# Kernel optimization log

Measured on AMD Instinct MI355X. Metric: run time of the kernel, lower is better.

The kernel has to match this reference:

```python
import jax, jax.numpy as jnp
import numpy as np

B, T, W, D, NT = 32, 512, 250, 768, 2  # batch, subtokens, words, sim_dim, num_tags


def setup_inputs() -> dict:
    key = jax.random.key(0)
    ks = jax.random.split(key, 20)
    s = 0.05
    # words_ids: 2 subtokens per word for W words, rest padding (-100)
    pos = jnp.arange(T)
    wid = jnp.where(pos < 2 * W, pos // 2, -100).astype(jnp.int64)
    words_ids = jnp.broadcast_to(wid, (B, T))
    inp = {
        'bert_out': jax.random.normal(ks[0], (B, T, D), jnp.float32),
        'words_ids': words_ids,
        'label_detect': jax.random.randint(ks[1], (B, W), 0, NT).astype(jnp.int64),
        'w_ih_l0': jax.random.normal(ks[2], (4 * D, D), jnp.float32) * s,
        'w_hh_l0': jax.random.normal(ks[3], (4 * D, D), jnp.float32) * s,
        'b_l0': jax.random.normal(ks[4], (4 * D,), jnp.float32) * s,
        'w_ih_l0r': jax.random.normal(ks[5], (4 * D, D), jnp.float32) * s,
        'w_hh_l0r': jax.random.normal(ks[6], (4 * D, D), jnp.float32) * s,
        'b_l0r': jax.random.normal(ks[7], (4 * D,), jnp.float32) * s,
        'w_ih_l1': jax.random.normal(ks[8], (4 * D, 2 * D), jnp.float32) * s,
        'w_hh_l1': jax.random.normal(ks[9], (4 * D, D), jnp.float32) * s,
        'b_l1': jax.random.normal(ks[10], (4 * D,), jnp.float32) * s,
        'w_ih_l1r': jax.random.normal(ks[11], (4 * D, 2 * D), jnp.float32) * s,
        'w_hh_l1r': jax.random.normal(ks[12], (4 * D, D), jnp.float32) * s,
        'b_l1r': jax.random.normal(ks[13], (4 * D,), jnp.float32) * s,
        'w_lin': jax.random.normal(ks[14], (NT, 2 * D), jnp.float32) * s,
        'b_lin': jax.random.normal(ks[15], (NT,), jnp.float32) * s,
        'crf_start': jax.random.normal(ks[16], (NT,), jnp.float32) * 0.1,
        'crf_end': jax.random.normal(ks[17], (NT,), jnp.float32) * 0.1,
        'crf_trans': jax.random.normal(ks[18], (NT, NT), jnp.float32) * 0.1,
    }
    return inp


def first_subtoken_gather(bert_out, words_ids):
    # For each word w in [0, W): embedding of its FIRST subtoken.
    # (matches torch.unique(sorted)+first-element-per-group on HF word_ids)
    pos = jnp.arange(T)
    mask = words_ids[:, None, :] == jnp.arange(W)[None, :, None]  # [B, W, T]
    first_idx = jnp.min(jnp.where(mask, pos[None, None, :], T - 1), axis=-1)  # [B, W]
    return jnp.take_along_axis(bert_out, first_idx[..., None], axis=1)  # [B, W, D]


def lstm_dir(x, w_ih, w_hh, b, reverse):
    # x: [B, S, In] -> [B, S, H]; PyTorch gate order i, f, g, o
    H = w_hh.shape[1]
    pre = jnp.einsum('bsi,gi->bsg', x, w_ih) + b  # b = b_ih + b_hh
    if reverse:
        pre = pre[:, ::-1]
    def step(carry, p_t):
        h, c = carry
        g = p_t + h @ w_hh.T
        i, f, gg, o = jnp.split(g, 4, axis=-1)
        c = jax.nn.sigmoid(f) * c + jax.nn.sigmoid(i) * jnp.tanh(gg)
        h = jax.nn.sigmoid(o) * jnp.tanh(c)
        return (h, c), h
    h0 = jnp.zeros((x.shape[0], H), x.dtype)
    _, hs = jax.lax.scan(step, (h0, h0), jnp.swapaxes(pre, 0, 1))
    hs = jnp.swapaxes(hs, 0, 1)
    if reverse:
        hs = hs[:, ::-1]
    return hs


def crf_log_likelihood(emis, tags, start, end, trans):
    # emis: [B, S, K]; tags: [B, S]; mask = all ones; reduction='mean'
    S = emis.shape[1]
    # numerator
    t0 = tags[:, 0]
    emis_score = jnp.sum(jnp.take_along_axis(emis, tags[..., None], axis=-1)[..., 0], axis=1)
    trans_score = jnp.sum(trans[tags[:, :-1], tags[:, 1:]], axis=1)
    num = start[t0] + emis_score + trans_score + end[tags[:, -1]]
    # partition (forward algorithm)
    alpha0 = start[None, :] + emis[:, 0]  # [B, K]
    def step(alpha, e_t):
        alpha = jax.nn.logsumexp(alpha[:, :, None] + trans[None] + e_t[:, None, :], axis=1)
        return alpha, None
    alpha, _ = jax.lax.scan(step, alpha0, jnp.swapaxes(emis[:, 1:], 0, 1))
    logZ = jax.nn.logsumexp(alpha + end[None, :], axis=-1)
    return jnp.mean(num - logZ)


def crf_decode(emis, start, end, trans):
    # Viterbi, mask = all ones. Returns [B, S] int32.
    score0 = start[None, :] + emis[:, 0]
    def fwd(score, e_t):
        cand = score[:, :, None] + trans[None]          # [B, K, K]
        bp = jnp.argmax(cand, axis=1)                    # [B, K]
        score = jnp.max(cand, axis=1) + e_t
        return score, bp
    score, hist = jax.lax.scan(fwd, score0, jnp.swapaxes(emis[:, 1:], 0, 1))
    last = jnp.argmax(score + end[None, :], axis=-1)     # [B]
    def back(tag, bp_t):
        prev = jnp.take_along_axis(bp_t, tag[:, None], axis=1)[:, 0]
        return prev, prev
    _, prevs = jax.lax.scan(back, last, hist, reverse=True)
    path = jnp.concatenate([jnp.swapaxes(prevs, 0, 1), last[:, None]], axis=1)
    return path.astype(jnp.int32)


def reference(bert_out, words_ids, label_detect,
              w_ih_l0, w_hh_l0, b_l0, w_ih_l0r, w_hh_l0r, b_l0r,
              w_ih_l1, w_hh_l1, b_l1, w_ih_l1r, w_hh_l1r, b_l1r,
              w_lin, b_lin, crf_start, crf_end, crf_trans):
    feat = first_subtoken_gather(bert_out, words_ids)                      # [B, W, D]
    h1 = jnp.concatenate([lstm_dir(feat, w_ih_l0, w_hh_l0, b_l0, False),
                          lstm_dir(feat, w_ih_l0r, w_hh_l0r, b_l0r, True)], axis=-1)
    h2 = jnp.concatenate([lstm_dir(h1, w_ih_l1, w_hh_l1, b_l1, False),
                          lstm_dir(h1, w_ih_l1r, w_hh_l1r, b_l1r, True)], axis=-1)
    logits = h2 @ w_lin.T + b_lin                                           # [B, W, 2]
    ner_prob = jax.nn.softmax(logits, axis=-1)
    llh = crf_log_likelihood(ner_prob, label_detect, crf_start, crf_end, crf_trans)
    path = crf_decode(ner_prob, crf_start, crf_end, crf_trans)
    loss = -1.0 * llh
    return path, ner_prob, loss
```

## Files before the change

kernel.cpp:

```cpp
#include <hip/hip_runtime.h>
#include <cmath>

#define B_ 32
#define T_ 512
#define W_ 250
#define D_ 768
#define H_ 768
#define G_ 3072
#define NT_ 2

#define NBAR_ 1152

__global__ void first_idx_kernel(const int* __restrict__ words_ids, int* __restrict__ fidx,
                                 unsigned int* __restrict__ counter) {
  int i = blockIdx.x * blockDim.x + threadIdx.x;
  if (i < NBAR_) counter[i] = 0u;
  if (i >= B_ * W_) return;
  int b = i / W_, w = i % W_;
  const int* row = words_ids + (size_t)b * T_;
  int idx = T_ - 1;
  for (int t = 0; t < T_; ++t) {
    if (row[t] == w) { idx = t; break; }
  }
  fidx[i] = idx;
}

__global__ void gather_kernel(const float* __restrict__ bert_out, const int* __restrict__ fidx,
                              float* __restrict__ feat) {
  int i = blockIdx.x * blockDim.x + threadIdx.x;
  const int nv = D_ / 4;
  if (i >= B_ * W_ * nv) return;
  int bw = i / nv, d4 = i % nv;
  int b = bw / W_, w = bw % W_;
  int t = fidx[bw];
  float4 v = ((const float4*)(bert_out + ((size_t)b * T_ + t) * D_))[d4];
  ((float4*)(feat + ((size_t)w * B_ + b) * D_))[d4] = v;
}

__global__ __launch_bounds__(256) void gemm_bias_kernel(
    const float* __restrict__ A, const float* __restrict__ Bm,
    const float* __restrict__ bias, float* __restrict__ C,
    int M, int N, int K) {
  __shared__ float As[2][16][132];
  __shared__ float Bs[2][16][132];
  const int tid = threadIdx.x;
  const int row0 = blockIdx.x * 128;
  const int col0 = blockIdx.y * 128;
  const int tx = tid & 15;
  const int ty = tid >> 4;
  const int lr = tid >> 1;
  const int lk = (tid & 1) * 8;

  int ar = row0 + lr;
  if (ar >= M) ar = M - 1;
  const float* __restrict__ Ap = A + (size_t)ar * K + lk;
  const float* __restrict__ Bp = Bm + (size_t)(col0 + lr) * K + lk;

  float acc[8][8];
#pragma unroll
  for (int i = 0; i < 8; ++i)
#pragma unroll
    for (int j = 0; j < 8; ++j) acc[i][j] = 0.0f;

  const int nk = K >> 4;

  {
    float4 a0 = *(const float4*)(Ap + 0);
    float4 a1 = *(const float4*)(Ap + 4);
    float4 b0 = *(const float4*)(Bp + 0);
    float4 b1 = *(const float4*)(Bp + 4);
    As[0][lk + 0][lr] = a0.x; As[0][lk + 1][lr] = a0.y; As[0][lk + 2][lr] = a0.z; As[0][lk + 3][lr] = a0.w;
    As[0][lk + 4][lr] = a1.x; As[0][lk + 5][lr] = a1.y; As[0][lk + 6][lr] = a1.z; As[0][lk + 7][lr] = a1.w;
    Bs[0][lk + 0][lr] = b0.x; Bs[0][lk + 1][lr] = b0.y; Bs[0][lk + 2][lr] = b0.z; Bs[0][lk + 3][lr] = b0.w;
    Bs[0][lk + 4][lr] = b1.x; Bs[0][lk + 5][lr] = b1.y; Bs[0][lk + 6][lr] = b1.z; Bs[0][lk + 7][lr] = b1.w;
  }
  __syncthreads();

  for (int t = 0; t < nk; ++t) {
    const int cur = t & 1;
    float4 a0, a1, b0, b1;
    const bool pf = (t + 1 < nk);
    if (pf) {
      const int k0 = (t + 1) << 4;
      a0 = *(const float4*)(Ap + k0);
      a1 = *(const float4*)(Ap + k0 + 4);
      b0 = *(const float4*)(Bp + k0);
      b1 = *(const float4*)(Bp + k0 + 4);
    }
#pragma unroll
    for (int k = 0; k < 16; ++k) {
      float a[8], b[8];
      *(float4*)&a[0] = *(const float4*)&As[cur][k][ty * 8];
      *(float4*)&a[4] = *(const float4*)&As[cur][k][ty * 8 + 4];
      *(float4*)&b[0] = *(const float4*)&Bs[cur][k][tx * 8];
      *(float4*)&b[4] = *(const float4*)&Bs[cur][k][tx * 8 + 4];
#pragma unroll
      for (int i = 0; i < 8; ++i)
#pragma unroll
        for (int j = 0; j < 8; ++j) acc[i][j] += a[i] * b[j];
    }
    if (pf) {
      const int nxt = cur ^ 1;
      As[nxt][lk + 0][lr] = a0.x; As[nxt][lk + 1][lr] = a0.y; As[nxt][lk + 2][lr] = a0.z; As[nxt][lk + 3][lr] = a0.w;
      As[nxt][lk + 4][lr] = a1.x; As[nxt][lk + 5][lr] = a1.y; As[nxt][lk + 6][lr] = a1.z; As[nxt][lk + 7][lr] = a1.w;
      Bs[nxt][lk + 0][lr] = b0.x; Bs[nxt][lk + 1][lr] = b0.y; Bs[nxt][lk + 2][lr] = b0.z; Bs[nxt][lk + 3][lr] = b0.w;
      Bs[nxt][lk + 4][lr] = b1.x; Bs[nxt][lk + 5][lr] = b1.y; Bs[nxt][lk + 6][lr] = b1.z; Bs[nxt][lk + 7][lr] = b1.w;
    }
    __syncthreads();
  }

#pragma unroll
  for (int i = 0; i < 8; ++i) {
    int r = row0 + ty * 8 + i;
    if (r < M) {
#pragma unroll
      for (int j = 0; j < 8; ++j) {
        int c = col0 + tx * 8 + j;
        C[(size_t)r * N + c] = acc[i][j] + bias[c];
      }
    }
  }
}

__global__ __launch_bounds__(256) void lstm_persist_kernel(
    const float* __restrict__ pre_f, const float* __restrict__ pre_r,
    const float* __restrict__ whh_f, const float* __restrict__ whh_r,
    float* __restrict__ out, float* __restrict__ hbuf, float* __restrict__ cbuf,
    unsigned int* __restrict__ counter, int s0, int Cc, int ep0) {
  const int wg = blockIdx.x;
  const int dir = wg >> 7;
  const int lw = wg & 127;
  const float* __restrict__ pre = dir ? pre_r : pre_f;
  const float* __restrict__ whh = dir ? whh_r : whh_f;
  float* hb = hbuf + (size_t)dir * 2 * B_ * H_;
  float* cb = cbuf + (size_t)dir * B_ * H_;
  const int tid = threadIdx.x;
  const int u0 = lw * 6;

  const int rgrp = tid >> 6;
  const int lane = tid & 63;
  const int kgrp = lane >> 3;
  const int bgrp = lane & 7;

  __shared__ float w_lds[24 * 860];
  __shared__ float h_lds[32 * 284];
  __shared__ float g_lds[32][24];

  unsigned int* __restrict__ grp  = counter + ((wg & 7) << 6);
  unsigned int* __restrict__ root = counter + 512;
  unsigned int* __restrict__ gow  = counter + 576 + ((wg & 7) << 6);

#pragma unroll
  for (int v = 0; v < 18; ++v) {
    int i = v * 256 + tid;
    int r24 = i / 192;
    int f4 = i - r24 * 192;
    int k = f4 * 4;
    int grow = (r24 / 6) * H_ + u0 + (r24 % 6);
    *(float4*)&w_lds[r24 * 860 + k + 4 * (k >> 5)] =
        *(const float4*)(whh + (size_t)grow * H_ + k);
  }

  const int cui = tid >> 5;
  const int cb_ = tid & 31;
  float creg = 0.0f;
  if (tid < 192 && s0 > 0) creg = cb[(size_t)cb_ * H_ + u0 + cui];

  float pre_g0 = 0.f, pre_g1 = 0.f, pre_g2 = 0.f, pre_g3 = 0.f;
  if (tid < 192) {
    const int prow0 = dir ? (Cc - 1) : 0;
    const float* pbt = pre + ((size_t)prow0 * B_ + cb_) * G_;
    pre_g0 = pbt[0 * H_ + u0 + cui];
    pre_g1 = pbt[1 * H_ + u0 + cui];
    pre_g2 = pbt[2 * H_ + u0 + cui];
    pre_g3 = pbt[3 * H_ + u0 + cui];
  }

  const int kl0 = kgrp * 32;

  for (int sl = 0; sl < Cc; ++sl) {
    const int s = s0 + sl;
    const int w = dir ? (W_ - 1 - s) : s;

    float acc[6][4];
#pragma unroll
    for (int r = 0; r < 6; ++r)
#pragma unroll
      for (int j = 0; j < 4; ++j) acc[r][j] = 0.0f;

    if (s > 0) {
      const float* __restrict__ hprev = hb + (size_t)(s & 1) * B_ * H_;

      unsigned long long hq[16];
#pragma unroll
      for (int v = 0; v < 8; ++v) {
        int e = v * 1024 + tid * 4;
        int bb = e >> 8;
        int kk = e & 255;
        const unsigned long long* src =
            (const unsigned long long*)(hprev + (size_t)bb * H_ + kk);
        hq[2 * v]     = __hip_atomic_load(src + 0, __ATOMIC_RELAXED, __HIP_MEMORY_SCOPE_AGENT);
        hq[2 * v + 1] = __hip_atomic_load(src + 1, __ATOMIC_RELAXED, __HIP_MEMORY_SCOPE_AGENT);
      }

      for (int kc = 0; kc < H_; kc += 256) {
        __syncthreads();
#pragma unroll
        for (int v = 0; v < 8; ++v) {
          int e = v * 1024 + tid * 4;
          int bb = e >> 8;
          int kk = e & 255;
          int off = bb * 284 + kk + 4 * (kk >> 5);
          union { unsigned long long u; float f[2]; } q0, q1;
          q0.u = hq[2 * v]; q1.u = hq[2 * v + 1];
          h_lds[off + 0] = q0.f[0]; h_lds[off + 1] = q0.f[1];
          h_lds[off + 2] = q1.f[0]; h_lds[off + 3] = q1.f[1];
        }
        __syncthreads();
        if (kc + 256 < H_) {
#pragma unroll
          for (int v = 0; v < 8; ++v) {
            int e = v * 1024 + tid * 4;
            int bb = e >> 8;
            int kk = e & 255;
            const unsigned long long* src =
                (const unsigned long long*)(hprev + (size_t)bb * H_ + kc + 256 + kk);
            hq[2 * v]     = __hip_atomic_load(src + 0, __ATOMIC_RELAXED, __HIP_MEMORY_SCOPE_AGENT);
            hq[2 * v + 1] = __hip_atomic_load(src + 1, __ATOMIC_RELAXED, __HIP_MEMORY_SCOPE_AGENT);
          }
        }

        const int wbase = kc + kl0;
#pragma unroll 4
        for (int t = 0; t < 8; ++t) {
          const int kl = kl0 + t * 4;
          const int ka = wbase + t * 4;
          const int hoff = kl + 4 * (kl >> 5);
          const int woff = ka + 4 * (ka >> 5);
          float4 h4_0 = *(const float4*)&h_lds[(4 * bgrp + 0) * 284 + hoff];
          float4 h4_1 = *(const float4*)&h_lds[(4 * bgrp + 1) * 284 + hoff];
          float4 h4_2 = *(const float4*)&h_lds[(4 * bgrp + 2) * 284 + hoff];
          float4 h4_3 = *(const float4*)&h_lds[(4 * bgrp + 3) * 284 + hoff];
#pragma unroll
          for (int r = 0; r < 6; ++r) {
            float4 w4 = *(const float4*)&w_lds[(rgrp * 6 + r) * 860 + woff];
            acc[r][0] += h4_0.x * w4.x + h4_0.y * w4.y + h4_0.z * w4.z + h4_0.w * w4.w;
            acc[r][1] += h4_1.x * w4.x + h4_1.y * w4.y + h4_1.z * w4.z + h4_1.w * w4.w;
            acc[r][2] += h4_2.x * w4.x + h4_2.y * w4.y + h4_2.z * w4.z + h4_2.w * w4.w;
            acc[r][3] += h4_3.x * w4.x + h4_3.y * w4.y + h4_3.z * w4.z + h4_3.w * w4.w;
          }
        }
      }

#pragma unroll
      for (int r = 0; r < 6; ++r)
#pragma unroll
        for (int j = 0; j < 4; ++j) {
          float a = acc[r][j];
          a += __shfl_xor(a, 8, 64);
          a += __shfl_xor(a, 16, 64);
          a += __shfl_xor(a, 32, 64);
          acc[r][j] = a;
        }
      if (kgrp == 0) {
#pragma unroll
        for (int r = 0; r < 6; ++r)
#pragma unroll
          for (int j = 0; j < 4; ++j)
            g_lds[4 * bgrp + j][rgrp * 6 + r] = acc[r][j];
      }
    }

    __syncthreads();

    if (tid < 192) {
      float gi = pre_g0, gf = pre_g1, gg = pre_g2, go = pre_g3;
      if (s > 0) {
        gi += g_lds[cb_][cui];
        gf += g_lds[cb_][6 + cui];
        gg += g_lds[cb_][12 + cui];
        go += g_lds[cb_][18 + cui];
      }
      const float si = 1.0f / (1.0f + expf(-gi));
      const float sf = 1.0f / (1.0f + expf(-gf));
      const float so = 1.0f / (1.0f + expf(-go));
      creg = sf * creg + si * tanhf(gg);
      const float h = so * tanhf(creg);
      float* __restrict__ hnext = hb + (size_t)((s + 1) & 1) * B_ * H_;
      __hip_atomic_store(&hnext[(size_t)cb_ * H_ + u0 + cui], h,
                         __ATOMIC_RELAXED, __HIP_MEMORY_SCOPE_AGENT);
      out[((size_t)w * B_ + cb_) * (2 * H_) + (size_t)dir * H_ + u0 + cui] = h;
      if (sl + 1 < Cc) {
        const int prown = dir ? (Cc - 2 - sl) : (sl + 1);
        const float* pbtn = pre + ((size_t)prown * B_ + cb_) * G_;
        pre_g0 = pbtn[0 * H_ + u0 + cui];
        pre_g1 = pbtn[1 * H_ + u0 + cui];
        pre_g2 = pbtn[2 * H_ + u0 + cui];
        pre_g3 = pbtn[3 * H_ + u0 + cui];
      }
    }

    __syncthreads();
    if (tid == 0) {
      const unsigned int ep1 = (unsigned int)(ep0 + sl + 1);
      unsigned int old = __hip_atomic_fetch_add(grp, 1u, __ATOMIC_RELAXED, __HIP_MEMORY_SCOPE_AGENT);
      if (old == 32u * ep1 - 1u) {
        __hip_atomic_fetch_add(root, 1u, __ATOMIC_RELAXED, __HIP_MEMORY_SCOPE_AGENT);
        while (__hip_atomic_load(root, __ATOMIC_RELAXED, __HIP_MEMORY_SCOPE_AGENT) < 8u * ep1) {
          __builtin_amdgcn_s_sleep(2);
        }
        __hip_atomic_store(gow, ep1, __ATOMIC_RELAXED, __HIP_MEMORY_SCOPE_AGENT);
      } else {
        while (__hip_atomic_load(gow, __ATOMIC_RELAXED, __HIP_MEMORY_SCOPE_AGENT) < ep1) {
          __builtin_amdgcn_s_sleep(2);
        }
      }
    }
    __syncthreads();
  }

  if (tid < 192) cb[(size_t)cb_ * H_ + u0 + cui] = creg;
}

__global__ void logits_softmax_kernel(const float* __restrict__ h2, const float* __restrict__ w_lin,
                                      const float* __restrict__ b_lin, float* __restrict__ prob) {
  int i = blockIdx.x * blockDim.x + threadIdx.x;
  if (i >= B_ * W_) return;
  int b = i / W_, w = i % W_;
  const float4* x = (const float4*)(h2 + ((size_t)w * B_ + b) * (2 * H_));
  const float4* w0 = (const float4*)(w_lin);
  const float4* w1 = (const float4*)(w_lin + 2 * H_);
  float l0 = 0.f, l1 = 0.f;
#pragma unroll 4
  for (int k = 0; k < (2 * H_) / 4; ++k) {
    float4 xv = x[k];
    float4 a = w0[k];
    float4 c = w1[k];
    l0 += xv.x * a.x + xv.y * a.y + xv.z * a.z + xv.w * a.w;
    l1 += xv.x * c.x + xv.y * c.y + xv.z * c.z + xv.w * c.w;
  }
  l0 += b_lin[0];
  l1 += b_lin[1];
  float m = fmaxf(l0, l1);
  float e0 = expf(l0 - m), e1 = expf(l1 - m);
  float s = e0 + e1;
  prob[2 * (size_t)i] = e0 / s;
  prob[2 * (size_t)i + 1] = e1 / s;
}

__device__ __forceinline__ float lse2(float a, float b) {
  float m = fmaxf(a, b);
  return m + logf(expf(a - m) + expf(b - m));
}

__global__ void crf_llh_kernel(const float* __restrict__ emis, const int* __restrict__ tags,
                               const float* __restrict__ start, const float* __restrict__ endv,
                               const float* __restrict__ trans, float* __restrict__ loss_out) {
  int tid = threadIdx.x;
  float val = 0.f;
  if (tid < B_) {
    const float* e = emis + (size_t)tid * W_ * NT_;
    const int* tg = tags + (size_t)tid * W_;
    const float t00 = trans[0], t01 = trans[1], t10 = trans[2], t11 = trans[3];
    int tp = tg[0];
    float num = start[tp] + e[tp];
    float a0 = start[0] + e[0];
    float a1 = start[1] + e[1];
    for (int s = 1; s < W_; ++s) {
      int ts = tg[s];
      num += e[2 * s + ts] + trans[tp * 2 + ts];
      tp = ts;
      float n0 = lse2(a0 + t00, a1 + t10) + e[2 * s];
      float n1 = lse2(a0 + t01, a1 + t11) + e[2 * s + 1];
      a0 = n0;
      a1 = n1;
    }
    num += endv[tp];
    float logZ = lse2(a0 + endv[0], a1 + endv[1]);
    val = num - logZ;
  }
  for (int off = 32; off > 0; off >>= 1) val += __shfl_down(val, off, 64);
  if (tid == 0) loss_out[0] = -(val / (float)B_);
}

__global__ void crf_decode_kernel(const float* __restrict__ emis,
                                  const float* __restrict__ start, const float* __restrict__ endv,
                                  const float* __restrict__ trans, float* __restrict__ path_out) {
  int b = blockIdx.x * blockDim.x + threadIdx.x;
  if (b >= B_) return;
  const float* e = emis + (size_t)b * W_ * NT_;
  const float t00 = trans[0], t01 = trans[1], t10 = trans[2], t11 = trans[3];
  float s0 = start[0] + e[0];
  float s1 = start[1] + e[1];
  unsigned long long bp0[4] = {0ull, 0ull, 0ull, 0ull};
  unsigned long long bp1[4] = {0ull, 0ull, 0ull, 0ull};
  for (int s = 1; s < W_; ++s) {
    float c00 = s0 + t00, c10 = s1 + t10;
    float c01 = s0 + t01, c11 = s1 + t11;
    int b0 = (c10 > c00) ? 1 : 0;
    int b1 = (c11 > c01) ? 1 : 0;
    float m0 = b0 ? c10 : c00;
    float m1 = b1 ? c11 : c01;
    int idx = s - 1;
    bp0[idx >> 6] |= ((unsigned long long)b0) << (idx & 63);
    bp1[idx >> 6] |= ((unsigned long long)b1) << (idx & 63);
    s0 = m0 + e[2 * s];
    s1 = m1 + e[2 * s + 1];
  }
  int tag = ((s1 + endv[1]) > (s0 + endv[0])) ? 1 : 0;
  path_out[(size_t)b * W_ + (W_ - 1)] = (float)tag;
  for (int s = W_ - 2; s >= 0; --s) {
    unsigned long long word = tag ? bp1[s >> 6] : bp0[s >> 6];
    tag = (int)((word >> (s & 63)) & 1ull);
    path_out[(size_t)b * W_ + s] = (float)tag;
  }
}

extern "C" void kernel_launch(void* const* d_in, const int* in_sizes, int n_in,
                              void* d_out, int out_size, void* d_ws, size_t ws_size,
                              hipStream_t stream) {
  const float* bert_out = (const float*)d_in[0];
  const int* words_ids = (const int*)d_in[1];
  const int* label_detect = (const int*)d_in[2];
  const float* w_ih_l0 = (const float*)d_in[3];
  const float* w_hh_l0 = (const float*)d_in[4];
  const float* b_l0 = (const float*)d_in[5];
  const float* w_ih_l0r = (const float*)d_in[6];
  const float* w_hh_l0r = (const float*)d_in[7];
  const float* b_l0r = (const float*)d_in[8];
  const float* w_ih_l1 = (const float*)d_in[9];
  const float* w_hh_l1 = (const float*)d_in[10];
  const float* b_l1 = (const float*)d_in[11];
  const float* w_ih_l1r = (const float*)d_in[12];
  const float* w_hh_l1r = (const float*)d_in[13];
  const float* b_l1r = (const float*)d_in[14];
  const float* w_lin = (const float*)d_in[15];
  const float* b_lin = (const float*)d_in[16];
  const float* crf_start = (const float*)d_in[17];
  const float* crf_end = (const float*)d_in[18];
  const float* crf_trans = (const float*)d_in[19];

  float* out = (float*)d_out;
  float* path_out = out;
  float* prob_out = out + B_ * W_;
  float* loss_out = out + B_ * W_ * 3;

  auto need = [](int c) -> size_t { return 4ull * (24732672ull + 196608ull * (size_t)c); };
  int C = 10;
  if (ws_size >= need(250)) C = 250;
  else if (ws_size >= need(125)) C = 125;
  else if (ws_size >= need(50)) C = 50;
  else if (ws_size >= need(25)) C = 25;
  const int nchunk = W_ / C;
  const size_t CBG = (size_t)C * B_ * G_;

  float* h2 = (float*)d_ws;
  float* feat = h2;
  float* h1 = h2 + 12288000;
  float* preA = h1 + 12288000;
  float* preB = preA + CBG;
  float* hbuf = preB + CBG;
  float* cbuf = hbuf + 2 * 2 * B_ * H_;
  int* fidx = (int*)(cbuf + 2 * B_ * H_);
  unsigned int* counter = (unsigned int*)(fidx + B_ * W_);

  first_idx_kernel<<<(B_ * W_ + 255) / 256, 256, 0, stream>>>(words_ids, fidx, counter);
  gather_kernel<<<(B_ * W_ * (D_ / 4) + 255) / 256, 256, 0, stream>>>(bert_out, fidx, feat);

  const int Mc = C * B_;
  dim3 ggrid((Mc + 127) / 128, G_ / 128);
  int ep = 0;

  for (int ch = 0; ch < nchunk; ++ch) {
    const int s0 = ch * C;
    gemm_bias_kernel<<<ggrid, 256, 0, stream>>>(feat + (size_t)s0 * B_ * D_, w_ih_l0, b_l0, preA, Mc, G_, D_);
    gemm_bias_kernel<<<ggrid, 256, 0, stream>>>(feat + (size_t)(W_ - C - s0) * B_ * D_, w_ih_l0r, b_l0r, preB, Mc, G_, D_);
    const float* a0 = preA; const float* a1 = preB;
    const float* a2 = w_hh_l0; const float* a3 = w_hh_l0r;
    float* a4 = h1; float* a5 = hbuf; float* a6 = cbuf;
    unsigned int* a7 = counter; int a8 = s0; int a9 = C; int a10 = ep;
    void* args[] = {&a0, &a1, &a2, &a3, &a4, &a5, &a6, &a7, &a8, &a9, &a10};
    hipLaunchCooperativeKernel((void*)lstm_persist_kernel, dim3(256), dim3(256), args, 0, stream);
    ep += C;
  }

  for (int ch = 0; ch < nchunk; ++ch) {
    const int s0 = ch * C;
    gemm_bias_kernel<<<ggrid, 256, 0, stream>>>(h1 + (size_t)s0 * B_ * (2 * H_), w_ih_l1, b_l1, preA, Mc, G_, 2 * H_);
    gemm_bias_kernel<<<ggrid, 256, 0, stream>>>(h1 + (size_t)(W_ - C - s0) * B_ * (2 * H_), w_ih_l1r, b_l1r, preB, Mc, G_, 2 * H_);
    const float* a0 = preA; const float* a1 = preB;
    const float* a2 = w_hh_l1; const float* a3 = w_hh_l1r;
    float* a4 = h2; float* a5 = hbuf; float* a6 = cbuf;
    unsigned int* a7 = counter; int a8 = s0; int a9 = C; int a10 = ep;
    void* args[] = {&a0, &a1, &a2, &a3, &a4, &a5, &a6, &a7, &a8, &a9, &a10};
    hipLaunchCooperativeKernel((void*)lstm_persist_kernel, dim3(256), dim3(256), args, 0, stream);
    ep += C;
  }

  logits_softmax_kernel<<<(B_ * W_ + 255) / 256, 256, 0, stream>>>(h2, w_lin, b_lin, prob_out);

  crf_llh_kernel<<<1, 64, 0, stream>>>(prob_out, label_detect, crf_start, crf_end, crf_trans, loss_out);
  crf_decode_kernel<<<1, 64, 0, stream>>>(prob_out, crf_start, crf_end, crf_trans, path_out);
}
```

Baseline: 10.81 ms.

## Spread persistent LSTM recurrence across 512 workgroups with three hidden units each

Adds a persistent LSTM kernel variant that runs 512 cooperative workgroups (256 per direction), each owning 3 hidden units instead of 6. Each workgroup holds a smaller slice of W_hh in LDS and does less matmul work per timestep, so every step of the serial recurrence should be shorter. The hierarchical grid barrier is widened to 16 groups and the counter area grows to match. The cost is twice as many workgroups taking part in each per-step barrier, and the variant needs 2 workgroups resident per CU. A runtime occupancy query picks it and falls back to the old kernel otherwise.

```diff
diff --git a/kernel.cpp b/kernel.cpp
--- a/kernel.cpp
+++ b/kernel.cpp
@@ -9,7 +9,7 @@
 #define G_ 3072
 #define NT_ 2
 
-#define NBAR_ 1152
+#define NBAR_ 2112
 
 __global__ void first_idx_kernel(const int* __restrict__ words_ids, int* __restrict__ fidx,
                                  unsigned int* __restrict__ counter) {
@@ -320,6 +320,206 @@
   }
 
   if (tid < 192) cb[(size_t)cb_ * H_ + u0 + cui] = creg;
+}
+
+__global__ __launch_bounds__(256) void lstm_persist512_kernel(
+    const float* __restrict__ pre_f, const float* __restrict__ pre_r,
+    const float* __restrict__ whh_f, const float* __restrict__ whh_r,
+    float* __restrict__ out, float* __restrict__ hbuf, float* __restrict__ cbuf,
+    unsigned int* __restrict__ counter, int s0, int Cc, int ep0) {
+  const int wg = blockIdx.x;
+  const int dir = wg >> 8;
+  const int lw = wg & 255;
+  const float* __restrict__ pre = dir ? pre_r : pre_f;
+  const float* __restrict__ whh = dir ? whh_r : whh_f;
+  float* hb = hbuf + (size_t)dir * 2 * B_ * H_;
+  float* cb = cbuf + (size_t)dir * B_ * H_;
+  const int tid = threadIdx.x;
+  const int u0 = lw * 3;
+
+  const int rgrp = tid >> 6;
+  const int lane = tid & 63;
+  const int kgrp = lane >> 3;
+  const int bgrp = lane & 7;
+
+  __shared__ float w_lds[12 * 860];
+  __shared__ float h_lds[32 * 284];
+  __shared__ float g_lds[32][12];
+
+  unsigned int* __restrict__ grp  = counter + ((wg & 15) << 6);
+  unsigned int* __restrict__ root = counter + 1024;
+  unsigned int* __restrict__ gow  = counter + 1088 + ((wg & 15) << 6);
+
+#pragma unroll
+  for (int v = 0; v < 9; ++v) {
+    int i = v * 256 + tid;
+    int r12 = i / 192;
+    int f4 = i - r12 * 192;
+    int k = f4 * 4;
+    int grow = (r12 / 3) * H_ + u0 + (r12 % 3);
+    *(float4*)&w_lds[r12 * 860 + k + 4 * (k >> 5)] =
+        *(const float4*)(whh + (size_t)grow * H_ + k);
+  }
+
+  const int cui = tid >> 5;
+  const int cb_ = tid & 31;
+  float creg = 0.0f;
+  if (tid < 96 && s0 > 0) creg = cb[(size_t)cb_ * H_ + u0 + cui];
+
+  float pre_g0 = 0.f, pre_g1 = 0.f, pre_g2 = 0.f, pre_g3 = 0.f;
+  if (tid < 96) {
+    const int prow0 = dir ? (Cc - 1) : 0;
+    const float* pbt = pre + ((size_t)prow0 * B_ + cb_) * G_;
+    pre_g0 = pbt[0 * H_ + u0 + cui];
+    pre_g1 = pbt[1 * H_ + u0 + cui];
+    pre_g2 = pbt[2 * H_ + u0 + cui];
+    pre_g3 = pbt[3 * H_ + u0 + cui];
+  }
+
+  const int kl0 = kgrp * 32;
+
+  for (int sl = 0; sl < Cc; ++sl) {
+    const int s = s0 + sl;
+    const int w = dir ? (W_ - 1 - s) : s;
+
+    float acc[3][4];
+#pragma unroll
+    for (int r = 0; r < 3; ++r)
+#pragma unroll
+      for (int j = 0; j < 4; ++j) acc[r][j] = 0.0f;
+
+    if (s > 0) {
+      const float* __restrict__ hprev = hb + (size_t)(s & 1) * B_ * H_;
+
+      unsigned long long hq[16];
+#pragma unroll
+      for (int v = 0; v < 8; ++v) {
+        int e = v * 1024 + tid * 4;
+        int bb = e >> 8;
+        int kk = e & 255;
+        const unsigned long long* src =
+            (const unsigned long long*)(hprev + (size_t)bb * H_ + kk);
+        hq[2 * v]     = __hip_atomic_load(src + 0, __ATOMIC_RELAXED, __HIP_MEMORY_SCOPE_AGENT);
+        hq[2 * v + 1] = __hip_atomic_load(src + 1, __ATOMIC_RELAXED, __HIP_MEMORY_SCOPE_AGENT);
+      }
+
+      for (int kc = 0; kc < H_; kc += 256) {
+        __syncthreads();
+#pragma unroll
+        for (int v = 0; v < 8; ++v) {
+          int e = v * 1024 + tid * 4;
+          int bb = e >> 8;
+          int kk = e & 255;
+          int off = bb * 284 + kk + 4 * (kk >> 5);
+          union { unsigned long long u; float f[2]; } q0, q1;
+          q0.u = hq[2 * v]; q1.u = hq[2 * v + 1];
+          h_lds[off + 0] = q0.f[0]; h_lds[off + 1] = q0.f[1];
+          h_lds[off + 2] = q1.f[0]; h_lds[off + 3] = q1.f[1];
+        }
+        __syncthreads();
+        if (kc + 256 < H_) {
+#pragma unroll
+          for (int v = 0; v < 8; ++v) {
+            int e = v * 1024 + tid * 4;
+            int bb = e >> 8;
+            int kk = e & 255;
+            const unsigned long long* src =
+                (const unsigned long long*)(hprev + (size_t)bb * H_ + kc + 256 + kk);
+            hq[2 * v]     = __hip_atomic_load(src + 0, __ATOMIC_RELAXED, __HIP_MEMORY_SCOPE_AGENT);
+            hq[2 * v + 1] = __hip_atomic_load(src + 1, __ATOMIC_RELAXED, __HIP_MEMORY_SCOPE_AGENT);
+          }
+        }
+
+        const int wbase = kc + kl0;
+#pragma unroll 4
+        for (int t = 0; t < 8; ++t) {
+          const int kl = kl0 + t * 4;
+          const int ka = wbase + t * 4;
+          const int hoff = kl + 4 * (kl >> 5);
+          const int woff = ka + 4 * (ka >> 5);
+          float4 h4_0 = *(const float4*)&h_lds[(4 * bgrp + 0) * 284 + hoff];
+          float4 h4_1 = *(const float4*)&h_lds[(4 * bgrp + 1) * 284 + hoff];
+          float4 h4_2 = *(const float4*)&h_lds[(4 * bgrp + 2) * 284 + hoff];
+          float4 h4_3 = *(const float4*)&h_lds[(4 * bgrp + 3) * 284 + hoff];
+#pragma unroll
+          for (int r = 0; r < 3; ++r) {
+            float4 w4 = *(const float4*)&w_lds[(rgrp * 3 + r) * 860 + woff];
+            acc[r][0] += h4_0.x * w4.x + h4_0.y * w4.y + h4_0.z * w4.z + h4_0.w * w4.w;
+            acc[r][1] += h4_1.x * w4.x + h4_1.y * w4.y + h4_1.z * w4.z + h4_1.w * w4.w;
+            acc[r][2] += h4_2.x * w4.x + h4_2.y * w4.y + h4_2.z * w4.z + h4_2.w * w4.w;
+            acc[r][3] += h4_3.x * w4.x + h4_3.y * w4.y + h4_3.z * w4.z + h4_3.w * w4.w;
+          }
+        }
+      }
+
+#pragma unroll
+      for (int r = 0; r < 3; ++r)
+#pragma unroll
+        for (int j = 0; j < 4; ++j) {
+          float a = acc[r][j];
+          a += __shfl_xor(a, 8, 64);
+          a += __shfl_xor(a, 16, 64);
+          a += __shfl_xor(a, 32, 64);
+          acc[r][j] = a;
+        }
+      if (kgrp == 0) {
+#pragma unroll
+        for (int r = 0; r < 3; ++r)
+#pragma unroll
+          for (int j = 0; j < 4; ++j)
+            g_lds[4 * bgrp + j][rgrp * 3 + r] = acc[r][j];
+      }
+    }
+
+    __syncthreads();
+
+    if (tid < 96) {
+      float gi = pre_g0, gf = pre_g1, gg = pre_g2, go = pre_g3;
+      if (s > 0) {
+        gi += g_lds[cb_][cui];
+        gf += g_lds[cb_][3 + cui];
+        gg += g_lds[cb_][6 + cui];
+        go += g_lds[cb_][9 + cui];
+      }
+      const float si = 1.0f / (1.0f + expf(-gi));
+      const float sf = 1.0f / (1.0f + expf(-gf));
+      const float so = 1.0f / (1.0f + expf(-go));
+      creg = sf * creg + si * tanhf(gg);
+      const float h = so * tanhf(creg);
+      float* __restrict__ hnext = hb + (size_t)((s + 1) & 1) * B_ * H_;
+      __hip_atomic_store(&hnext[(size_t)cb_ * H_ + u0 + cui], h,
+                         __ATOMIC_RELAXED, __HIP_MEMORY_SCOPE_AGENT);
+      out[((size_t)w * B_ + cb_) * (2 * H_) + (size_t)dir * H_ + u0 + cui] = h;
+      if (sl + 1 < Cc) {
+        const int prown = dir ? (Cc - 2 - sl) : (sl + 1);
+        const float* pbtn = pre + ((size_t)prown * B_ + cb_) * G_;
+        pre_g0 = pbtn[0 * H_ + u0 + cui];
+        pre_g1 = pbtn[1 * H_ + u0 + cui];
+        pre_g2 = pbtn[2 * H_ + u0 + cui];
+        pre_g3 = pbtn[3 * H_ + u0 + cui];
+      }
+    }
+
+    __syncthreads();
+    if (tid == 0) {
+      const unsigned int ep1 = (unsigned int)(ep0 + sl + 1);
+      unsigned int old = __hip_atomic_fetch_add(grp, 1u, __ATOMIC_RELAXED, __HIP_MEMORY_SCOPE_AGENT);
+      if (old == 32u * ep1 - 1u) {
+        __hip_atomic_fetch_add(root, 1u, __ATOMIC_RELAXED, __HIP_MEMORY_SCOPE_AGENT);
+        while (__hip_atomic_load(root, __ATOMIC_RELAXED, __HIP_MEMORY_SCOPE_AGENT) < 16u * ep1) {
+          __builtin_amdgcn_s_sleep(2);
+        }
+        __hip_atomic_store(gow, ep1, __ATOMIC_RELAXED, __HIP_MEMORY_SCOPE_AGENT);
+      } else {
+        while (__hip_atomic_load(gow, __ATOMIC_RELAXED, __HIP_MEMORY_SCOPE_AGENT) < ep1) {
+          __builtin_amdgcn_s_sleep(2);
+        }
+      }
+    }
+    __syncthreads();
+  }
+
+  if (tid < 96) cb[(size_t)cb_ * H_ + u0 + cui] = creg;
 }
 
 __global__ void logits_softmax_kernel(const float* __restrict__ h2, const float* __restrict__ w_lin,
@@ -445,7 +645,11 @@
   float* prob_out = out + B_ * W_;
   float* loss_out = out + B_ * W_ * 3;
 
-  auto need = [](int c) -> size_t { return 4ull * (24732672ull + 196608ull * (size_t)c); };
+  int occ512 = 0;
+  (void)hipOccupancyMaxActiveBlocksPerMultiprocessor(&occ512, (const void*)lstm_persist512_kernel, 256, 0);
+  const bool use512 = (occ512 >= 2);
+
+  auto need = [](int c) -> size_t { return 4ull * (24733568ull + 196608ull * (size_t)c); };
   int C = 10;
   if (ws_size >= need(250)) C = 250;
   else if (ws_size >= need(125)) C = 125;
@@ -471,6 +675,9 @@
   dim3 ggrid((Mc + 127) / 128, G_ / 128);
   int ep = 0;
 
+  void* lstm_fn = use512 ? (void*)lstm_persist512_kernel : (void*)lstm_persist_kernel;
+  const dim3 lstm_grid = use512 ? dim3(512) : dim3(256);
+
   for (int ch = 0; ch < nchunk; ++ch) {
     const int s0 = ch * C;
     gemm_bias_kernel<<<ggrid, 256, 0, stream>>>(feat + (size_t)s0 * B_ * D_, w_ih_l0, b_l0, preA, Mc, G_, D_);
@@ -480,7 +687,7 @@
     float* a4 = h1; float* a5 = hbuf; float* a6 = cbuf;
     unsigned int* a7 = counter; int a8 = s0; int a9 = C; int a10 = ep;
     void* args[] = {&a0, &a1, &a2, &a3, &a4, &a5, &a6, &a7, &a8, &a9, &a10};
-    hipLaunchCooperativeKernel((void*)lstm_persist_kernel, dim3(256), dim3(256), args, 0, stream);
+    hipLaunchCooperativeKernel(lstm_fn, lstm_grid, dim3(256), args, 0, stream);
     ep += C;
   }
 
@@ -493,7 +700,7 @@
     float* a4 = h2; float* a5 = hbuf; float* a6 = cbuf;
     unsigned int* a7 = counter; int a8 = s0; int a9 = C; int a10 = ep;
     void* args[] = {&a0, &a1, &a2, &a3, &a4, &a5, &a6, &a7, &a8, &a9, &a10};
-    hipLaunchCooperativeKernel((void*)lstm_persist_kernel, dim3(256), dim3(256), args, 0, stream);
+    hipLaunchCooperativeKernel(lstm_fn, lstm_grid, dim3(256), args, 0, stream);
     ep += C;
   }
 
```

New measurement: 10.88 ms. Within noise of the previous version (+0.6%).
